# Optimization experiments

Measured on AMD Instinct MI355X. Metric: run time of the kernel, lower is better.

The kernel has to match this reference:

```python
import jax, jax.numpy as jnp
import numpy as np

FACTOR = 5  # init arg 'factor'


def setup_inputs() -> dict:
    key = jax.random.key(0)
    ks = jax.random.split(key, 9)
    B, L, H, D = 32, 4096, 8, 64
    sh = (B, L, H, D)
    scale = 0.125  # 1/sqrt(D)
    return {
        "queries": jax.random.normal(ks[0], sh, jnp.float32),
        "keys": jax.random.normal(ks[1], sh, jnp.float32),
        "values": jax.random.normal(ks[2], sh, jnp.float32),
        "Wq": jax.random.normal(ks[3], (1, D), jnp.float32) * scale,
        "bq": jax.random.normal(ks[4], (1,), jnp.float32) * scale,
        "Wk": jax.random.normal(ks[5], (1, D), jnp.float32) * scale,
        "bk": jax.random.normal(ks[6], (1,), jnp.float32) * scale,
        "Wv": jax.random.normal(ks[7], (1, D), jnp.float32) * scale,
        "bv": jax.random.normal(ks[8], (1,), jnp.float32) * scale,
    }


def reference(queries, keys, values, Wq, bq, Wk, bk, Wv, bv):
    B, L_Q, H, D = queries.shape
    # transpose(2,1) + LazyLinear(1) + squeeze  ->  scalar series per (b, h, t)
    q = jnp.einsum('blhd,d->bhl', queries, Wq[0]) + bq[0]  # [B,H,L_Q]
    k = jnp.einsum('blhd,d->bhl', keys, Wk[0]) + bk[0]
    v = jnp.einsum('blhd,d->bhl', values, Wv[0]) + bv[0]
    # L_K == L_Q here: torch takes the last L_Q steps (identity in this config)
    k = k[:, :, -L_Q:]
    v = v[:, :, -L_Q:]
    # FFT cross-correlation scores (rfft with n=2L-1 -> L bins; irfft default -> 2L-2)
    n_fft = 2 * L_Q - 1
    Qf = jnp.fft.rfft(q, n_fft)
    Kf = jnp.conj(jnp.fft.rfft(k, n_fft))
    score = jnp.fft.irfft(Qf * Kf)[:, :, :L_Q] / L_Q  # [B,H,L_Q]
    kk = FACTOR * int(np.ceil(np.log(L_Q)))  # 45 for L_Q=4096
    weight, top_idx = jax.lax.top_k(score, kk)  # [B,H,kk]
    weight = jax.nn.softmax(weight, axis=-1)
    # torch: indices = L_Q - top_idx - 1; rolled-V row j is roll(v, j+1),
    # i.e. shift = L_Q - top_idx, so V_sel[b,h,d,t] = v[b,h,(t + top_idx[b,h,d]) % L_Q].
    t = jnp.arange(L_Q)
    gidx = (top_idx[..., None] + t[None, None, None, :]) % L_Q  # [B,H,kk,L_Q]
    V_sel = jnp.take_along_axis(v[:, :, None, :], gidx, axis=-1)  # [B,H,kk,L_Q]
    out = jnp.einsum('bhd,bhdl->bhl', weight, V_sel)  # [B,H,L_Q]
    return out[..., None]  # [B,H,L_Q,1]
```

## Files before the change

### kernel.cpp

```cpp
#include <hip/hip_runtime.h>
#include <math.h>
#include <float.h>

#define L_   4096
#define M_   8192
#define H_   8
#define D_   64
#define KK   45

#define WS_C   0
#define WS_D   4096
#define WS_TW  8192
#define WS_H1  16384
#define WS_H2  24576
#define WS_QKV 32768

__device__ __forceinline__ float2 cadd(float2 a, float2 b) { return make_float2(a.x + b.x, a.y + b.y); }
__device__ __forceinline__ float2 csub(float2 a, float2 b) { return make_float2(a.x - b.x, a.y - b.y); }
__device__ __forceinline__ float2 cmulf(float2 a, float2 b) {
  return make_float2(a.x * b.x - a.y * b.y, a.x * b.y + a.y * b.x);
}
__device__ __forceinline__ float2 cmulcf(float2 a, float2 b) {
  return make_float2(a.x * b.x + a.y * b.y, a.y * b.x - a.x * b.y);
}

__device__ __forceinline__ float2 twf(int e) {
  float s, c;
  __sincosf((float)e * -7.66990394e-4f, &s, &c);
  return make_float2(c, s);
}

#define R4DIF(BUF) { \
  const float2 a = BUF[i0], b = BUF[i0 + q], c = BUF[i0 + 2 * q], d = BUF[i0 + 3 * q]; \
  const float2 t0 = cadd(a, c), t1 = csub(a, c), t2 = cadd(b, d), t3 = csub(b, d); \
  BUF[i0]         = cadd(t0, t2); \
  BUF[i0 + q]     = cmulf(make_float2(t1.x + t3.y, t1.y - t3.x), w1); \
  BUF[i0 + 2 * q] = cmulf(csub(t0, t2), w2); \
  BUF[i0 + 3 * q] = cmulf(make_float2(t1.x - t3.y, t1.y + t3.x), w3); }

#define R4DIT(BUF) { \
  const float2 z0 = BUF[i0]; \
  const float2 z1 = cmulcf(BUF[i0 + q],     w1); \
  const float2 z2 = cmulcf(BUF[i0 + 2 * q], w2); \
  const float2 z3 = cmulcf(BUF[i0 + 3 * q], w3); \
  const float2 t0 = cadd(z0, z2), t1 = csub(z0, z2), t2 = cadd(z1, z3), u = csub(z1, z3); \
  BUF[i0]         = cadd(t0, t2); \
  BUF[i0 + q]     = make_float2(t1.x - u.y, t1.y + u.x); \
  BUF[i0 + 2 * q] = csub(t0, t2); \
  BUF[i0 + 3 * q] = make_float2(t1.x + u.y, t1.y - u.x); }

__device__ __forceinline__ float4 midpair(float4 a, float4 h) {
  float2 u = make_float2(a.x + a.z, a.y + a.w);
  float2 v = make_float2(a.x - a.z, a.y - a.w);
  u = cmulf(u, make_float2(h.x, h.y));
  v = cmulf(v, make_float2(h.z, h.w));
  return make_float4(u.x + v.x, u.y + v.y, u.x - v.x, u.y - v.y);
}

static __device__ void conv2(float2* A, float2* B, const float2* __restrict__ Hf) {
  const int tid = threadIdx.x;
  #pragma unroll
  for (int s = 0; s < 6; ++s) {
    const int q = 2048 >> (2 * s);
    __syncthreads();
    #pragma unroll
    for (int r = 0; r < 2; ++r) {
      const int bid = tid + (r << 10);
      const int j   = bid & (q - 1);
      const int i0  = ((bid >> (11 - 2 * s)) << (13 - 2 * s)) + j;
      const float2 w1 = twf(j << (2 * s));
      const float2 w2 = cmulf(w1, w1);
      const float2 w3 = cmulf(w2, w1);
      R4DIF(A) R4DIF(B)
    }
  }
  __syncthreads();
  #pragma unroll
  for (int r = 0; r < 4; ++r) {
    const int p = tid + (r << 10);
    const float4 h = reinterpret_cast<const float4*>(Hf)[p];
    reinterpret_cast<float4*>(A)[p] = midpair(reinterpret_cast<float4*>(A)[p], h);
    reinterpret_cast<float4*>(B)[p] = midpair(reinterpret_cast<float4*>(B)[p], h);
  }
  #pragma unroll
  for (int s = 5; s >= 0; --s) {
    const int q = 2048 >> (2 * s);
    __syncthreads();
    #pragma unroll
    for (int r = 0; r < 2; ++r) {
      const int bid = tid + (r << 10);
      const int j   = bid & (q - 1);
      const int i0  = ((bid >> (11 - 2 * s)) << (13 - 2 * s)) + j;
      const float2 w1 = twf(j << (2 * s));
      const float2 w2 = cmulf(w1, w1);
      const float2 w3 = cmulf(w2, w1);
      R4DIT(A) R4DIT(B)
    }
  }
  __syncthreads();
}

static __device__ void conv1(float2* A, const float2* __restrict__ Hf) {
  const int tid = threadIdx.x;
  #pragma unroll
  for (int s = 0; s < 6; ++s) {
    const int q = 2048 >> (2 * s);
    __syncthreads();
    #pragma unroll
    for (int r = 0; r < 2; ++r) {
      const int bid = tid + (r << 10);
      const int j   = bid & (q - 1);
      const int i0  = ((bid >> (11 - 2 * s)) << (13 - 2 * s)) + j;
      const float2 w1 = twf(j << (2 * s));
      const float2 w2 = cmulf(w1, w1);
      const float2 w3 = cmulf(w2, w1);
      R4DIF(A)
    }
  }
  __syncthreads();
  #pragma unroll
  for (int r = 0; r < 4; ++r) {
    const int p = tid + (r << 10);
    const float4 h = reinterpret_cast<const float4*>(Hf)[p];
    reinterpret_cast<float4*>(A)[p] = midpair(reinterpret_cast<float4*>(A)[p], h);
  }
  #pragma unroll
  for (int s = 5; s >= 0; --s) {
    const int q = 2048 >> (2 * s);
    __syncthreads();
    #pragma unroll
    for (int r = 0; r < 2; ++r) {
      const int bid = tid + (r << 10);
      const int j   = bid & (q - 1);
      const int i0  = ((bid >> (11 - 2 * s)) << (13 - 2 * s)) + j;
      const float2 w1 = twf(j << (2 * s));
      const float2 w2 = cmulf(w1, w1);
      const float2 w3 = cmulf(w2, w1);
      R4DIT(A)
    }
  }
  __syncthreads();
}

template <int NT>
static __device__ void fft_dif_tab(float2* buf, const float2* __restrict__ tw) {
  const int tid = threadIdx.x;
  for (int s = 0; s < 6; ++s) {
    const int q = 2048 >> (2 * s);
    __syncthreads();
    for (int r = 0; r < 2048 / NT; ++r) {
      const int bid = tid + r * NT;
      const int j   = bid & (q - 1);
      const int i0  = ((bid >> (11 - 2 * s)) << (13 - 2 * s)) + j;
      const int e   = j << (2 * s);
      const float2 w1 = tw[e], w2 = tw[2 * e], w3 = tw[3 * e];
      R4DIF(buf)
    }
  }
  __syncthreads();
  for (int r = 0; r < 4096 / NT; ++r) {
    const int i0 = (tid + r * NT) << 1;
    const float2 a = buf[i0], b = buf[i0 + 1];
    buf[i0] = cadd(a, b); buf[i0 + 1] = csub(a, b);
  }
  __syncthreads();
}

extern "C" __global__ void setup_tables(float2* ws) {
  const int idx = blockIdx.x * 512 + threadIdx.x;
  if (idx < 4096) {
    const long p = ((long)idx * idx) % 16382;
    const double th = -M_PI * (double)p / 8191.0;
    double s, c; sincos(th, &s, &c);
    ws[WS_C + idx] = make_float2((float)c, (float)s);
  } else if (idx < 8192) {
    const int j = idx - 4096;
    const long p = ((long)j * j) % 16380;
    const double th = M_PI * (double)p / 8190.0;
    double s, c; sincos(th, &s, &c);
    ws[WS_D + j] = make_float2((float)c, (float)s);
  } else if (idx < 16384) {
    const int j = idx - 8192;
    const double th = -M_PI * (double)j / 4096.0;
    double s, c; sincos(th, &s, &c);
    ws[WS_TW + j] = make_float2((float)c, (float)s);
  }
}

extern "C" __global__ __launch_bounds__(512, 1) void setup_filters(float2* ws) {
  __shared__ __align__(16) float2 buf[M_];
  const float2* src = ws + (blockIdx.x == 0 ? WS_C : WS_D);
  float2*       dst = ws + (blockIdx.x == 0 ? WS_H1 : WS_H2);
  const float2* tw  = ws + WS_TW;
  for (int i = threadIdx.x; i < M_; i += 512) {
    float2 val = make_float2(0.f, 0.f);
    if (i != 4096) {
      const int jj = (i <= 4095) ? i : (M_ - i);
      const float2 e = src[jj];
      val = make_float2(e.x, -e.y);
    }
    buf[i] = val;
  }
  fft_dif_tab<512>(buf, tw);
  const float sc = 1.0f / 8192.0f;
  for (int i = threadIdx.x; i < M_; i += 512)
    dst[i] = make_float2(buf[i].x * sc, buf[i].y * sc);
}

#define PROJ_ISSUE(BUF, IT) { \
  const int s_ = (IT) >> 3, g_ = (IT) & 7; \
  const int l0_ = lbase + (wave << 1) + (g_ << 3); \
  const float4* p_ = (s_ == 0 ? q4p : (s_ == 1 ? k4p : v4p)) + (((size_t)l0_) << 7) + (lane << 2); \
  BUF[0] = p_[0]; \
  BUF[1] = p_[1]; \
  BUF[2] = p_[2]; \
  BUF[3] = p_[3]; }

#define PROJ_REDUCE(BUF, IT) { \
  const int s_ = (IT) >> 3, g_ = (IT) & 7; \
  const int l0_ = lbase + (wave << 1) + (g_ << 3); \
  const float4 w0_ = (s_ == 0 ? wq0 : (s_ == 1 ? wk0 : wv0)); \
  const float4 w1_ = (s_ == 0 ? wq1 : (s_ == 1 ? wk1 : wv1)); \
  const float4 w2_ = (s_ == 0 ? wq2 : (s_ == 1 ? wk2 : wv2)); \
  const float4 w3_ = (s_ == 0 ? wq3 : (s_ == 1 ? wk3 : wv3)); \
  float f_ = BUF[0].x * w0_.x + BUF[0].y * w0_.y + BUF[0].z * w0_.z + BUF[0].w * w0_.w \
           + BUF[1].x * w1_.x + BUF[1].y * w1_.y + BUF[1].z * w1_.z + BUF[1].w * w1_.w \
           + BUF[2].x * w2_.x + BUF[2].y * w2_.y + BUF[2].z * w2_.z + BUF[2].w * w2_.w \
           + BUF[3].x * w3_.x + BUF[3].y * w3_.y + BUF[3].z * w3_.z + BUF[3].w * w3_.w; \
  f_ += __shfl_xor(f_, 1); f_ += __shfl_xor(f_, 2); \
  if (qt == 0) { \
    float* d_ = (s_ == 0 ? q_ws : (s_ == 1 ? k_ws : v_ws)) + (((size_t)(b8 + hh)) << 12) + l0_ + dl; \
    *d_ = f_ + (s_ == 0 ? bq0 : (s_ == 1 ? bk0 : bv0)); } }

extern "C" __global__ __launch_bounds__(256, 4)
void proj_kernel(const float* __restrict__ queries, const float* __restrict__ keys,
                 const float* __restrict__ values,
                 const float* __restrict__ Wq, const float* __restrict__ bq,
                 const float* __restrict__ Wk, const float* __restrict__ bk,
                 const float* __restrict__ Wv, const float* __restrict__ bv,
                 float* __restrict__ q_ws, float* __restrict__ k_ws,
                 float* __restrict__ v_ws)
{
  const int tid  = threadIdx.x;
  const int wave = tid >> 6;
  const int lane = tid & 63;
  const int qt   = lane & 3;
  const int rr   = lane >> 2;
  const int hh   = rr & 7;
  const int dl   = rr >> 3;
  const int blk  = blockIdx.x;
  const int b    = blk >> 6;
  const int b8   = b * 8;
  const int lbase = (blk & 63) << 6;

  const float4* q4p = reinterpret_cast<const float4*>(queries) + (size_t)b * 524288;
  const float4* k4p = reinterpret_cast<const float4*>(keys)    + (size_t)b * 524288;
  const float4* v4p = reinterpret_cast<const float4*>(values)  + (size_t)b * 524288;

  const float4* Wq4 = reinterpret_cast<const float4*>(Wq);
  const float4* Wk4 = reinterpret_cast<const float4*>(Wk);
  const float4* Wv4 = reinterpret_cast<const float4*>(Wv);
  const float4 wq0 = Wq4[qt * 4 + 0], wq1 = Wq4[qt * 4 + 1], wq2 = Wq4[qt * 4 + 2], wq3 = Wq4[qt * 4 + 3];
  const float4 wk0 = Wk4[qt * 4 + 0], wk1 = Wk4[qt * 4 + 1], wk2 = Wk4[qt * 4 + 2], wk3 = Wk4[qt * 4 + 3];
  const float4 wv0 = Wv4[qt * 4 + 0], wv1 = Wv4[qt * 4 + 1], wv2 = Wv4[qt * 4 + 2], wv3 = Wv4[qt * 4 + 3];
  const float bq0 = bq[0], bk0 = bk[0], bv0 = bv[0];

  float4 bA[4], bB[4], bC[4];
  PROJ_ISSUE(bA, 0)
  PROJ_ISSUE(bB, 1)
  #pragma unroll
  for (int it = 0; it < 24; ++it) {
    const int nx = it + 2;
    if (nx < 24) {
      if      (nx % 3 == 0) { PROJ_ISSUE(bA, nx) }
      else if (nx % 3 == 1) { PROJ_ISSUE(bB, nx) }
      else                  { PROJ_ISSUE(bC, nx) }
    }
    if      (it % 3 == 0) { PROJ_REDUCE(bA, it) }
    else if (it % 3 == 1) { PROJ_REDUCE(bB, it) }
    else                  { PROJ_REDUCE(bC, it) }
  }
}

extern "C" __global__ __launch_bounds__(1024, 1)
void autocorr_main(const float2* __restrict__ ws,
                   const float* __restrict__ q_ws, const float* __restrict__ k_ws,
                   const float* __restrict__ v_ws, float* __restrict__ outp)
{
  __shared__ __align__(16) float2 bufA[M_];
  __shared__ __align__(16) float2 bufB[M_];
  __shared__ float  v_lds[L_];
  __shared__ float  cand_v[16 * KK];
  __shared__ int    cand_i[16 * KK];
  __shared__ float  w_sh[KK];
  __shared__ int    i_sh[KK];

  const int tid = threadIdx.x;
  const int bh  = blockIdx.x;

  const float2* c_t = ws + WS_C;
  const float2* d_t = ws + WS_D;
  const float2* H1  = ws + WS_H1;
  const float2* H2  = ws + WS_H2;
  const float* qrow = q_ws + ((size_t)bh << 12);
  const float* krow = k_ws + ((size_t)bh << 12);
  const float* vrow = v_ws + ((size_t)bh << 12);

  {
    const float4 v4 = reinterpret_cast<const float4*>(vrow)[tid];
    reinterpret_cast<float4*>(v_lds)[tid] = v4;
    const float4 k4 = reinterpret_cast<const float4*>(krow)[tid];
    const float4 q4 = reinterpret_cast<const float4*>(qrow)[tid];
    const float4 c01 = reinterpret_cast<const float4*>(c_t)[2 * tid];
    const float4 c23 = reinterpret_cast<const float4*>(c_t)[2 * tid + 1];
    float4* A4 = reinterpret_cast<float4*>(bufA);
    float4* B4 = reinterpret_cast<float4*>(bufB);
    A4[2 * tid]     = make_float4(k4.x * c01.x, k4.x * c01.y, k4.y * c01.z, k4.y * c01.w);
    A4[2 * tid + 1] = make_float4(k4.z * c23.x, k4.z * c23.y, k4.w * c23.z, k4.w * c23.w);
    B4[2 * tid]     = make_float4(q4.x * c01.x, q4.x * c01.y, q4.y * c01.z, q4.y * c01.w);
    B4[2 * tid + 1] = make_float4(q4.z * c23.x, q4.z * c23.y, q4.w * c23.z, q4.w * c23.w);
    const float4 z = make_float4(0.f, 0.f, 0.f, 0.f);
    A4[2048 + tid] = z; A4[3072 + tid] = z;
    B4[2048 + tid] = z; B4[3072 + tid] = z;
  }

  conv2(bufA, bufB, H1);

  #pragma unroll
  for (int r = 0; r < 4; ++r) {
    const int m = tid + (r << 10);
    const float2 cc = c_t[m];
    const float2 K = cmulf(cc, bufA[m]);
    const float2 Q = cmulf(cc, bufB[m]);
    const float2 F = cmulcf(Q, K);
    float2 g;
    if (m == 0 || m == 4095) g = make_float2(F.x, 0.f);
    else                     g = make_float2(2.f * F.x, 2.f * F.y);
    bufA[m] = cmulf(g, d_t[m]);
  }
  #pragma unroll
  for (int r = 4; r < 8; ++r) bufA[tid + (r << 10)] = make_float2(0.f, 0.f);

  conv1(bufA, H2);

  const float SCALE = (float)(1.0 / (8190.0 * 4096.0));
  float svv[4]; int sii[4];
  #pragma unroll
  for (int r = 0; r < 4; ++r) {
    const int t = tid + (r << 10);
    const float2 Z = cmulf(d_t[t], bufA[t]);
    svv[r] = Z.x * SCALE;
    sii[r] = t;
  }
  const int lane = tid & 63, wv = tid >> 6;
  for (int it = 0; it < KK; ++it) {
    float bvv = -FLT_MAX; int bii = 0x7fffffff;
    #pragma unroll
    for (int c = 0; c < 4; ++c)
      if (svv[c] > bvv || (svv[c] == bvv && sii[c] < bii)) { bvv = svv[c]; bii = sii[c]; }
    #pragma unroll
    for (int off = 1; off < 64; off <<= 1) {
      const float ov = __shfl_xor(bvv, off);
      const int   oi = __shfl_xor(bii, off);
      if (ov > bvv || (ov == bvv && oi < bii)) { bvv = ov; bii = oi; }
    }
    #pragma unroll
    for (int c = 0; c < 4; ++c) if (sii[c] == bii) svv[c] = -FLT_MAX;
    if (lane == 0) { cand_v[wv * KK + it] = bvv; cand_i[wv * KK + it] = bii; }
  }
  __syncthreads();

  if (tid < 64) {
    float mv[12]; int mi[12];
    #pragma unroll
    for (int c = 0; c < 12; ++c) {
      const int id = tid + 64 * c;
      if (id < 16 * KK) { mv[c] = cand_v[id]; mi[c] = cand_i[id]; }
      else              { mv[c] = -FLT_MAX;   mi[c] = 0x7fffffff; }
    }
    float m0 = 0.f, sum = 0.f, myv = -FLT_MAX; int myi = 0;
    for (int it = 0; it < KK; ++it) {
      float bvv = -FLT_MAX; int bii = 0x7fffffff;
      #pragma unroll
      for (int c = 0; c < 12; ++c)
        if (mv[c] > bvv || (mv[c] == bvv && mi[c] < bii)) { bvv = mv[c]; bii = mi[c]; }
      #pragma unroll
      for (int off = 1; off < 64; off <<= 1) {
        const float ov = __shfl_xor(bvv, off);
        const int   oi = __shfl_xor(bii, off);
        if (ov > bvv || (ov == bvv && oi < bii)) { bvv = ov; bii = oi; }
      }
      if (it == 0) m0 = bvv;
      sum += expf(bvv - m0);
      if (tid == it) { myv = bvv; myi = bii; }
      #pragma unroll
      for (int c = 0; c < 12; ++c) if (mi[c] == bii) mv[c] = -FLT_MAX;
    }
    if (tid < KK) { w_sh[tid] = expf(myv - m0) / sum; i_sh[tid] = myi; }
  }
  __syncthreads();

  {
    float acc[4] = {0, 0, 0, 0};
    for (int j = 0; j < KK; ++j) {
      const float wj = w_sh[j];
      const int   bse = i_sh[j] + tid;
      #pragma unroll
      for (int r = 0; r < 4; ++r)
        acc[r] = fmaf(wj, v_lds[(bse + (r << 10)) & (L_ - 1)], acc[r]);
    }
    float* op = outp + ((size_t)bh << 12);
    #pragma unroll
    for (int r = 0; r < 4; ++r) op[tid + (r << 10)] = acc[r];
  }
}

extern "C" void kernel_launch(void* const* d_in, const int* in_sizes, int n_in,
                              void* d_out, int out_size, void* d_ws, size_t ws_size,
                              hipStream_t stream) {
  const float* queries = (const float*)d_in[0];
  const float* keys    = (const float*)d_in[1];
  const float* values  = (const float*)d_in[2];
  const float* Wq = (const float*)d_in[3];
  const float* bq = (const float*)d_in[4];
  const float* Wk = (const float*)d_in[5];
  const float* bk = (const float*)d_in[6];
  const float* Wv = (const float*)d_in[7];
  const float* bv = (const float*)d_in[8];
  float2* ws = (float2*)d_ws;
  float* q_ws = (float*)d_ws + 2 * WS_QKV;
  float* k_ws = q_ws + (1 << 20);
  float* v_ws = k_ws + (1 << 20);
  float* out = (float*)d_out;

  hipLaunchKernelGGL(setup_tables,  dim3(32), dim3(512), 0, stream, ws);
  hipLaunchKernelGGL(setup_filters, dim3(2),  dim3(512), 0, stream, ws);
  hipLaunchKernelGGL(proj_kernel,   dim3(2048), dim3(256), 0, stream,
                     queries, keys, values, Wq, bq, Wk, bk, Wv, bv, q_ws, k_ws, v_ws);
  hipLaunchKernelGGL(autocorr_main, dim3(256), dim3(1024), 0, stream,
                     ws, q_ws, k_ws, v_ws, out);
}
```

Before: 339.9 us.

## Replace radix-4 FFT convolutions with radix-8 stages and fused middle stage

Rewrites the Bluestein convolution FFTs from six radix-4 stages to three radix-8 stages plus a fused 'megamid' stage, which does the last radix-8 forward pass, the filter multiply and the first inverse pass in registers. The first forward stage is fused with loading the inputs and the chirp premultiply, and skips the known zero padding. This halves the number of shared-memory passes and __syncthreads barriers per convolution. Each thread holds more registers and uses more twiddle multiplies. The launch-bounds minimum-blocks hint also changes from 1 to 4.

```diff
diff --git a/kernel.cpp b/kernel.cpp
--- a/kernel.cpp
+++ b/kernel.cpp
@@ -30,140 +30,143 @@
   return make_float2(c, s);
 }
 
-#define R4DIF(BUF) { \
-  const float2 a = BUF[i0], b = BUF[i0 + q], c = BUF[i0 + 2 * q], d = BUF[i0 + 3 * q]; \
-  const float2 t0 = cadd(a, c), t1 = csub(a, c), t2 = cadd(b, d), t3 = csub(b, d); \
-  BUF[i0]         = cadd(t0, t2); \
-  BUF[i0 + q]     = cmulf(make_float2(t1.x + t3.y, t1.y - t3.x), w1); \
-  BUF[i0 + 2 * q] = cmulf(csub(t0, t2), w2); \
-  BUF[i0 + 3 * q] = cmulf(make_float2(t1.x - t3.y, t1.y + t3.x), w3); }
-
-#define R4DIT(BUF) { \
-  const float2 z0 = BUF[i0]; \
-  const float2 z1 = cmulcf(BUF[i0 + q],     w1); \
-  const float2 z2 = cmulcf(BUF[i0 + 2 * q], w2); \
-  const float2 z3 = cmulcf(BUF[i0 + 3 * q], w3); \
-  const float2 t0 = cadd(z0, z2), t1 = csub(z0, z2), t2 = cadd(z1, z3), u = csub(z1, z3); \
-  BUF[i0]         = cadd(t0, t2); \
-  BUF[i0 + q]     = make_float2(t1.x - u.y, t1.y + u.x); \
-  BUF[i0 + 2 * q] = csub(t0, t2); \
-  BUF[i0 + 3 * q] = make_float2(t1.x + u.y, t1.y - u.x); }
-
-__device__ __forceinline__ float4 midpair(float4 a, float4 h) {
-  float2 u = make_float2(a.x + a.z, a.y + a.w);
-  float2 v = make_float2(a.x - a.z, a.y - a.w);
-  u = cmulf(u, make_float2(h.x, h.y));
-  v = cmulf(v, make_float2(h.z, h.w));
-  return make_float4(u.x + v.x, u.y + v.y, u.x - v.x, u.y - v.y);
-}
-
-static __device__ void conv2(float2* A, float2* B, const float2* __restrict__ Hf) {
-  const int tid = threadIdx.x;
-  #pragma unroll
-  for (int s = 0; s < 6; ++s) {
-    const int q = 2048 >> (2 * s);
-    __syncthreads();
-    #pragma unroll
-    for (int r = 0; r < 2; ++r) {
-      const int bid = tid + (r << 10);
-      const int j   = bid & (q - 1);
-      const int i0  = ((bid >> (11 - 2 * s)) << (13 - 2 * s)) + j;
-      const float2 w1 = twf(j << (2 * s));
-      const float2 w2 = cmulf(w1, w1);
-      const float2 w3 = cmulf(w2, w1);
-      R4DIF(A) R4DIF(B)
-    }
-  }
-  __syncthreads();
-  #pragma unroll
-  for (int r = 0; r < 4; ++r) {
-    const int p = tid + (r << 10);
-    const float4 h = reinterpret_cast<const float4*>(Hf)[p];
-    reinterpret_cast<float4*>(A)[p] = midpair(reinterpret_cast<float4*>(A)[p], h);
-    reinterpret_cast<float4*>(B)[p] = midpair(reinterpret_cast<float4*>(B)[p], h);
-  }
-  #pragma unroll
-  for (int s = 5; s >= 0; --s) {
-    const int q = 2048 >> (2 * s);
-    __syncthreads();
-    #pragma unroll
-    for (int r = 0; r < 2; ++r) {
-      const int bid = tid + (r << 10);
-      const int j   = bid & (q - 1);
-      const int i0  = ((bid >> (11 - 2 * s)) << (13 - 2 * s)) + j;
-      const float2 w1 = twf(j << (2 * s));
-      const float2 w2 = cmulf(w1, w1);
-      const float2 w3 = cmulf(w2, w1);
-      R4DIT(A) R4DIT(B)
-    }
-  }
-  __syncthreads();
-}
-
-static __device__ void conv1(float2* A, const float2* __restrict__ Hf) {
-  const int tid = threadIdx.x;
-  #pragma unroll
-  for (int s = 0; s < 6; ++s) {
-    const int q = 2048 >> (2 * s);
-    __syncthreads();
-    #pragma unroll
-    for (int r = 0; r < 2; ++r) {
-      const int bid = tid + (r << 10);
-      const int j   = bid & (q - 1);
-      const int i0  = ((bid >> (11 - 2 * s)) << (13 - 2 * s)) + j;
-      const float2 w1 = twf(j << (2 * s));
-      const float2 w2 = cmulf(w1, w1);
-      const float2 w3 = cmulf(w2, w1);
-      R4DIF(A)
-    }
-  }
-  __syncthreads();
-  #pragma unroll
-  for (int r = 0; r < 4; ++r) {
-    const int p = tid + (r << 10);
-    const float4 h = reinterpret_cast<const float4*>(Hf)[p];
-    reinterpret_cast<float4*>(A)[p] = midpair(reinterpret_cast<float4*>(A)[p], h);
-  }
-  #pragma unroll
-  for (int s = 5; s >= 0; --s) {
-    const int q = 2048 >> (2 * s);
-    __syncthreads();
-    #pragma unroll
-    for (int r = 0; r < 2; ++r) {
-      const int bid = tid + (r << 10);
-      const int j   = bid & (q - 1);
-      const int i0  = ((bid >> (11 - 2 * s)) << (13 - 2 * s)) + j;
-      const float2 w1 = twf(j << (2 * s));
-      const float2 w2 = cmulf(w1, w1);
-      const float2 w3 = cmulf(w2, w1);
-      R4DIT(A)
-    }
-  }
-  __syncthreads();
-}
-
-template <int NT>
-static __device__ void fft_dif_tab(float2* buf, const float2* __restrict__ tw) {
-  const int tid = threadIdx.x;
-  for (int s = 0; s < 6; ++s) {
-    const int q = 2048 >> (2 * s);
-    __syncthreads();
-    for (int r = 0; r < 2048 / NT; ++r) {
-      const int bid = tid + r * NT;
-      const int j   = bid & (q - 1);
-      const int i0  = ((bid >> (11 - 2 * s)) << (13 - 2 * s)) + j;
-      const int e   = j << (2 * s);
-      const float2 w1 = tw[e], w2 = tw[2 * e], w3 = tw[3 * e];
-      R4DIF(buf)
-    }
-  }
-  __syncthreads();
-  for (int r = 0; r < 4096 / NT; ++r) {
-    const int i0 = (tid + r * NT) << 1;
-    const float2 a = buf[i0], b = buf[i0 + 1];
-    buf[i0] = cadd(a, b); buf[i0 + 1] = csub(a, b);
-  }
-  __syncthreads();
+__device__ __forceinline__ void mk_tw(int e, float2 w[8]) {
+  w[1] = twf(e);
+  w[2] = cmulf(w[1], w[1]);
+  w[3] = cmulf(w[2], w[1]);
+  w[4] = cmulf(w[2], w[2]);
+  w[5] = cmulf(w[4], w[1]);
+  w[6] = cmulf(w[3], w[3]);
+  w[7] = cmulf(w[4], w[3]);
+}
+
+__device__ __forceinline__ void bfly8_dif(float2 x[8]) {
+  const float2 a0 = cadd(x[0], x[4]), a1 = csub(x[0], x[4]);
+  const float2 a2 = cadd(x[2], x[6]), a3 = csub(x[2], x[6]);
+  const float2 a4 = cadd(x[1], x[5]), a5 = csub(x[1], x[5]);
+  const float2 a6 = cadd(x[3], x[7]), a7 = csub(x[3], x[7]);
+  const float2 b0 = cadd(a0, a2), b1 = csub(a0, a2);
+  const float2 b2 = cadd(a4, a6), b3 = csub(a4, a6);
+  const float s = 0.70710678118654752f;
+  const float2 c0 = make_float2(a1.x + a3.y, a1.y - a3.x);
+  const float2 c1 = make_float2(a1.x - a3.y, a1.y + a3.x);
+  const float2 c2 = make_float2(a5.x + a7.y, a5.y - a7.x);
+  const float2 c3 = make_float2(a5.x - a7.y, a5.y + a7.x);
+  const float2 t2 = make_float2(s * (c2.x + c2.y), s * (c2.y - c2.x));
+  const float2 t3 = make_float2(s * (c3.y - c3.x), -s * (c3.x + c3.y));
+  x[0] = cadd(b0, b2);
+  x[4] = csub(b0, b2);
+  x[2] = make_float2(b1.x + b3.y, b1.y - b3.x);
+  x[6] = make_float2(b1.x - b3.y, b1.y + b3.x);
+  x[1] = cadd(c0, t2);
+  x[5] = csub(c0, t2);
+  x[3] = cadd(c1, t3);
+  x[7] = csub(c1, t3);
+}
+
+__device__ __forceinline__ void bfly8_dit(float2 x[8]) {
+  const float2 a0 = cadd(x[0], x[4]), a1 = csub(x[0], x[4]);
+  const float2 a2 = cadd(x[2], x[6]), a3 = csub(x[2], x[6]);
+  const float2 a4 = cadd(x[1], x[5]), a5 = csub(x[1], x[5]);
+  const float2 a6 = cadd(x[3], x[7]), a7 = csub(x[3], x[7]);
+  const float2 b0 = cadd(a0, a2), b1 = csub(a0, a2);
+  const float2 b2 = cadd(a4, a6), b3 = csub(a4, a6);
+  const float s = 0.70710678118654752f;
+  const float2 c0 = make_float2(a1.x - a3.y, a1.y + a3.x);
+  const float2 c1 = make_float2(a1.x + a3.y, a1.y - a3.x);
+  const float2 c2 = make_float2(a5.x - a7.y, a5.y + a7.x);
+  const float2 c3 = make_float2(a5.x + a7.y, a5.y - a7.x);
+  const float2 t2 = make_float2(s * (c2.x - c2.y), s * (c2.x + c2.y));
+  const float2 t3 = make_float2(-s * (c3.x + c3.y), s * (c3.x - c3.y));
+  x[0] = cadd(b0, b2);
+  x[4] = csub(b0, b2);
+  x[2] = make_float2(b1.x - b3.y, b1.y + b3.x);
+  x[6] = make_float2(b1.x + b3.y, b1.y - b3.x);
+  x[1] = cadd(c0, t2);
+  x[5] = csub(c0, t2);
+  x[3] = cadd(c1, t3);
+  x[7] = csub(c1, t3);
+}
+
+#define C8f 0.923879532511287f
+#define S8f 0.382683432365090f
+#define Q8f 0.707106781186548f
+
+__device__ __forceinline__ void megamid(float2* T, const float2* __restrict__ Hf, int wk) {
+  float4* T4 = reinterpret_cast<float4*>(T);
+  const float4* H4 = reinterpret_cast<const float4*>(Hf);
+  const int b4 = wk << 3;
+  const int st = wk & 7;
+  float2 ev[8], od[8];
+  #pragma unroll
+  for (int mm = 0; mm < 8; ++mm) {
+    const int m = (mm + st) & 7;
+    const float4 t = T4[b4 + m];
+    ev[m] = make_float2(t.x, t.y);
+    od[m] = make_float2(t.z, t.w);
+  }
+  bfly8_dif(ev);
+  bfly8_dif(od);
+  od[1] = cmulf(od[1], make_float2(C8f, -S8f));
+  od[2] = cmulf(od[2], make_float2(Q8f, -Q8f));
+  od[3] = cmulf(od[3], make_float2(S8f, -C8f));
+  od[4] = make_float2(od[4].y, -od[4].x);
+  od[5] = cmulf(od[5], make_float2(-S8f, -C8f));
+  od[6] = cmulf(od[6], make_float2(-Q8f, -Q8f));
+  od[7] = cmulf(od[7], make_float2(-C8f, -S8f));
+  #pragma unroll
+  for (int m = 0; m < 8; ++m) {
+    const float4 h = H4[b4 + m];
+    float2 u = cadd(ev[m], od[m]);
+    float2 v = csub(ev[m], od[m]);
+    u = cmulf(u, make_float2(h.x, h.y));
+    v = cmulf(v, make_float2(h.z, h.w));
+    ev[m] = cadd(u, v);
+    od[m] = csub(u, v);
+  }
+  od[1] = cmulcf(od[1], make_float2(C8f, -S8f));
+  od[2] = cmulcf(od[2], make_float2(Q8f, -Q8f));
+  od[3] = cmulcf(od[3], make_float2(S8f, -C8f));
+  od[4] = make_float2(-od[4].y, od[4].x);
+  od[5] = cmulcf(od[5], make_float2(-S8f, -C8f));
+  od[6] = cmulcf(od[6], make_float2(-Q8f, -Q8f));
+  od[7] = cmulcf(od[7], make_float2(-C8f, -S8f));
+  bfly8_dit(ev);
+  bfly8_dit(od);
+  #pragma unroll
+  for (int mm = 0; mm < 8; ++mm) {
+    const int m = (mm + st) & 7;
+    T4[b4 + m] = make_float4(ev[m].x, ev[m].y, od[m].x, od[m].y);
+  }
+}
+
+__device__ __forceinline__ void r8_fwd_stage(float2* T, int s, int tid) {
+  const int q  = 1024 >> (3 * s);
+  const int j  = tid & (q - 1);
+  const int i0 = ((tid >> (10 - 3 * s)) << (13 - 3 * s)) + j;
+  float2 w[8]; mk_tw(j << (3 * s), w);
+  float2 x[8];
+  #pragma unroll
+  for (int k = 0; k < 8; ++k) x[k] = T[i0 + k * q];
+  bfly8_dif(x);
+  T[i0] = x[0];
+  #pragma unroll
+  for (int k = 1; k < 8; ++k) T[i0 + k * q] = cmulf(x[k], w[k]);
+}
+
+__device__ __forceinline__ void r8_inv_stage(float2* T, int s, int tid) {
+  const int q  = 1024 >> (3 * s);
+  const int j  = tid & (q - 1);
+  const int i0 = ((tid >> (10 - 3 * s)) << (13 - 3 * s)) + j;
+  float2 w[8]; mk_tw(j << (3 * s), w);
+  float2 x[8];
+  #pragma unroll
+  for (int k = 0; k < 8; ++k) x[k] = T[i0 + k * q];
+  #pragma unroll
+  for (int k = 1; k < 8; ++k) x[k] = cmulcf(x[k], w[k]);
+  bfly8_dit(x);
+  #pragma unroll
+  for (int k = 0; k < 8; ++k) T[i0 + k * q] = x[k];
 }
 
 extern "C" __global__ void setup_tables(float2* ws) {
@@ -187,6 +190,35 @@
   }
 }
 
+template <int NT>
+static __device__ void fft8_dif_tab(float2* buf, const float2* __restrict__ tw) {
+  const int tid = threadIdx.x;
+  for (int s = 0; s < 4; ++s) {
+    const int q = 1024 >> (3 * s);
+    __syncthreads();
+    for (int r = 0; r < 1024 / NT; ++r) {
+      const int bid = tid + r * NT;
+      const int j   = bid & (q - 1);
+      const int i0  = ((bid >> (10 - 3 * s)) << (13 - 3 * s)) + j;
+      const int e   = j << (3 * s);
+      float2 x[8];
+      #pragma unroll
+      for (int k = 0; k < 8; ++k) x[k] = buf[i0 + k * q];
+      bfly8_dif(x);
+      buf[i0] = x[0];
+      #pragma unroll
+      for (int k = 1; k < 8; ++k) buf[i0 + k * q] = cmulf(x[k], tw[k * e]);
+    }
+  }
+  __syncthreads();
+  for (int r = 0; r < 4096 / NT; ++r) {
+    const int i0 = (tid + r * NT) << 1;
+    const float2 a = buf[i0], b = buf[i0 + 1];
+    buf[i0] = cadd(a, b); buf[i0 + 1] = csub(a, b);
+  }
+  __syncthreads();
+}
+
 extern "C" __global__ __launch_bounds__(512, 1) void setup_filters(float2* ws) {
   __shared__ __align__(16) float2 buf[M_];
   const float2* src = ws + (blockIdx.x == 0 ? WS_C : WS_D);
@@ -201,7 +233,7 @@
     }
     buf[i] = val;
   }
-  fft_dif_tab<512>(buf, tw);
+  fft8_dif_tab<512>(buf, tw);
   const float sc = 1.0f / 8192.0f;
   for (int i = threadIdx.x; i < M_; i += 512)
     dst[i] = make_float2(buf[i].x * sc, buf[i].y * sc);
@@ -282,7 +314,7 @@
   }
 }
 
-extern "C" __global__ __launch_bounds__(1024, 1)
+extern "C" __global__ __launch_bounds__(1024, 4)
 void autocorr_main(const float2* __restrict__ ws,
                    const float* __restrict__ q_ws, const float* __restrict__ k_ws,
                    const float* __restrict__ v_ws, float* __restrict__ outp)
@@ -309,39 +341,81 @@
   {
     const float4 v4 = reinterpret_cast<const float4*>(vrow)[tid];
     reinterpret_cast<float4*>(v_lds)[tid] = v4;
-    const float4 k4 = reinterpret_cast<const float4*>(krow)[tid];
-    const float4 q4 = reinterpret_cast<const float4*>(qrow)[tid];
-    const float4 c01 = reinterpret_cast<const float4*>(c_t)[2 * tid];
-    const float4 c23 = reinterpret_cast<const float4*>(c_t)[2 * tid + 1];
-    float4* A4 = reinterpret_cast<float4*>(bufA);
-    float4* B4 = reinterpret_cast<float4*>(bufB);
-    A4[2 * tid]     = make_float4(k4.x * c01.x, k4.x * c01.y, k4.y * c01.z, k4.y * c01.w);
-    A4[2 * tid + 1] = make_float4(k4.z * c23.x, k4.z * c23.y, k4.w * c23.z, k4.w * c23.w);
-    B4[2 * tid]     = make_float4(q4.x * c01.x, q4.x * c01.y, q4.y * c01.z, q4.y * c01.w);
-    B4[2 * tid + 1] = make_float4(q4.z * c23.x, q4.z * c23.y, q4.w * c23.z, q4.w * c23.w);
-    const float4 z = make_float4(0.f, 0.f, 0.f, 0.f);
-    A4[2048 + tid] = z; A4[3072 + tid] = z;
-    B4[2048 + tid] = z; B4[3072 + tid] = z;
-  }
-
-  conv2(bufA, bufB, H1);
-
-  #pragma unroll
-  for (int r = 0; r < 4; ++r) {
-    const int m = tid + (r << 10);
-    const float2 cc = c_t[m];
-    const float2 K = cmulf(cc, bufA[m]);
-    const float2 Q = cmulf(cc, bufB[m]);
-    const float2 F = cmulcf(Q, K);
-    float2 g;
-    if (m == 0 || m == 4095) g = make_float2(F.x, 0.f);
-    else                     g = make_float2(2.f * F.x, 2.f * F.y);
-    bufA[m] = cmulf(g, d_t[m]);
-  }
-  #pragma unroll
-  for (int r = 4; r < 8; ++r) bufA[tid + (r << 10)] = make_float2(0.f, 0.f);
-
-  conv1(bufA, H2);
+  }
+
+  {
+    float2 w[8]; mk_tw(tid, w);
+    float2 xA[8], xB[8];
+    #pragma unroll
+    for (int k = 0; k < 4; ++k) {
+      const int m = tid + (k << 10);
+      const float2 cc = c_t[m];
+      const float kv = krow[m];
+      const float qv = qrow[m];
+      xA[k] = make_float2(kv * cc.x, kv * cc.y);
+      xB[k] = make_float2(qv * cc.x, qv * cc.y);
+    }
+    #pragma unroll
+    for (int k = 4; k < 8; ++k) { xA[k] = make_float2(0.f, 0.f); xB[k] = make_float2(0.f, 0.f); }
+    bfly8_dif(xA);
+    bfly8_dif(xB);
+    bufA[tid] = xA[0];
+    bufB[tid] = xB[0];
+    #pragma unroll
+    for (int k = 1; k < 8; ++k) {
+      bufA[tid + (k << 10)] = cmulf(xA[k], w[k]);
+      bufB[tid + (k << 10)] = cmulf(xB[k], w[k]);
+    }
+  }
+  __syncthreads();
+  r8_fwd_stage(bufA, 1, tid); r8_fwd_stage(bufB, 1, tid);
+  __syncthreads();
+  r8_fwd_stage(bufA, 2, tid); r8_fwd_stage(bufB, 2, tid);
+  __syncthreads();
+  megamid((tid >> 9) ? bufB : bufA, H1, tid & 511);
+  __syncthreads();
+  r8_inv_stage(bufA, 2, tid); r8_inv_stage(bufB, 2, tid);
+  __syncthreads();
+  r8_inv_stage(bufA, 1, tid); r8_inv_stage(bufB, 1, tid);
+  __syncthreads();
+  r8_inv_stage(bufA, 0, tid); r8_inv_stage(bufB, 0, tid);
+  __syncthreads();
+
+  {
+    float2 w[8]; mk_tw(tid, w);
+    float2 x[8];
+    #pragma unroll
+    for (int k = 0; k < 4; ++k) {
+      const int m = tid + (k << 10);
+      const float2 cc = c_t[m];
+      const float2 K = cmulf(cc, bufA[m]);
+      const float2 Q = cmulf(cc, bufB[m]);
+      const float2 F = cmulcf(Q, K);
+      float2 g;
+      if (m == 0 || m == 4095) g = make_float2(F.x, 0.f);
+      else                     g = make_float2(2.f * F.x, 2.f * F.y);
+      x[k] = cmulf(g, d_t[m]);
+    }
+    #pragma unroll
+    for (int k = 4; k < 8; ++k) x[k] = make_float2(0.f, 0.f);
+    bfly8_dif(x);
+    bufA[tid] = x[0];
+    #pragma unroll
+    for (int k = 1; k < 8; ++k) bufA[tid + (k << 10)] = cmulf(x[k], w[k]);
+  }
+  __syncthreads();
+  r8_fwd_stage(bufA, 1, tid);
+  __syncthreads();
+  r8_fwd_stage(bufA, 2, tid);
+  __syncthreads();
+  if (tid < 512) megamid(bufA, H2, tid);
+  __syncthreads();
+  r8_inv_stage(bufA, 2, tid);
+  __syncthreads();
+  r8_inv_stage(bufA, 1, tid);
+  __syncthreads();
+  r8_inv_stage(bufA, 0, tid);
+  __syncthreads();
 
   const float SCALE = (float)(1.0 / (8190.0 * 4096.0));
   float svv[4]; int sii[4];
```

Measured after the change: 413.3 us. +21.6%, slower.

## Fuse first and last radix-4 FFT stages into register-resident prologue and epilogue

Applied to the files above, without the earlier changes.

Peels the first DIF stage and the last DIT stage out of each Bluestein convolution and runs them in registers, fused with the chirp premultiply, the zero padding, the spectrum product, and the score extraction. Half of each butterfly's inputs are known zeros, so the peeled first stage skips those loads. The inverse pass only keeps the outputs that are needed. This cuts several shared-memory round trips, barriers and zero-fill stores per block. The cost is more register pressure, and the global loads of k and q become scalar instead of float4.

```diff
diff --git a/kernel.cpp b/kernel.cpp
--- a/kernel.cpp
+++ b/kernel.cpp
@@ -49,6 +49,26 @@
   BUF[i0 + 2 * q] = csub(t0, t2); \
   BUF[i0 + 3 * q] = make_float2(t1.x + u.y, t1.y - u.x); }
 
+__device__ __forceinline__ void bfly4_dif(float2 x[4], float2 w1, float2 w2, float2 w3) {
+  const float2 t0 = cadd(x[0], x[2]), t1 = csub(x[0], x[2]);
+  const float2 t2 = cadd(x[1], x[3]), t3 = csub(x[1], x[3]);
+  x[0] = cadd(t0, t2);
+  x[1] = cmulf(make_float2(t1.x + t3.y, t1.y - t3.x), w1);
+  x[2] = cmulf(csub(t0, t2), w2);
+  x[3] = cmulf(make_float2(t1.x - t3.y, t1.y + t3.x), w3);
+}
+__device__ __forceinline__ void bfly4_dit(float2 x[4], float2 w1, float2 w2, float2 w3) {
+  const float2 z0 = x[0];
+  const float2 z1 = cmulcf(x[1], w1);
+  const float2 z2 = cmulcf(x[2], w2);
+  const float2 z3 = cmulcf(x[3], w3);
+  const float2 t0 = cadd(z0, z2), t1 = csub(z0, z2), t2 = cadd(z1, z3), u = csub(z1, z3);
+  x[0] = cadd(t0, t2);
+  x[1] = make_float2(t1.x - u.y, t1.y + u.x);
+  x[2] = csub(t0, t2);
+  x[3] = make_float2(t1.x + u.y, t1.y - u.x);
+}
+
 __device__ __forceinline__ float4 midpair(float4 a, float4 h) {
   float2 u = make_float2(a.x + a.z, a.y + a.w);
   float2 v = make_float2(a.x - a.z, a.y - a.w);
@@ -57,10 +77,10 @@
   return make_float4(u.x + v.x, u.y + v.y, u.x - v.x, u.y - v.y);
 }
 
-static __device__ void conv2(float2* A, float2* B, const float2* __restrict__ Hf) {
+static __device__ void fwd_stages2(float2* A, float2* B) {
   const int tid = threadIdx.x;
   #pragma unroll
-  for (int s = 0; s < 6; ++s) {
+  for (int s = 1; s < 6; ++s) {
     const int q = 2048 >> (2 * s);
     __syncthreads();
     #pragma unroll
@@ -74,16 +94,11 @@
       R4DIF(A) R4DIF(B)
     }
   }
-  __syncthreads();
-  #pragma unroll
-  for (int r = 0; r < 4; ++r) {
-    const int p = tid + (r << 10);
-    const float4 h = reinterpret_cast<const float4*>(Hf)[p];
-    reinterpret_cast<float4*>(A)[p] = midpair(reinterpret_cast<float4*>(A)[p], h);
-    reinterpret_cast<float4*>(B)[p] = midpair(reinterpret_cast<float4*>(B)[p], h);
-  }
-  #pragma unroll
-  for (int s = 5; s >= 0; --s) {
+}
+static __device__ void inv_stages2(float2* A, float2* B) {
+  const int tid = threadIdx.x;
+  #pragma unroll
+  for (int s = 5; s >= 1; --s) {
     const int q = 2048 >> (2 * s);
     __syncthreads();
     #pragma unroll
@@ -97,13 +112,11 @@
       R4DIT(A) R4DIT(B)
     }
   }
-  __syncthreads();
-}
-
-static __device__ void conv1(float2* A, const float2* __restrict__ Hf) {
+}
+static __device__ void fwd_stages1(float2* A) {
   const int tid = threadIdx.x;
   #pragma unroll
-  for (int s = 0; s < 6; ++s) {
+  for (int s = 1; s < 6; ++s) {
     const int q = 2048 >> (2 * s);
     __syncthreads();
     #pragma unroll
@@ -117,15 +130,11 @@
       R4DIF(A)
     }
   }
-  __syncthreads();
-  #pragma unroll
-  for (int r = 0; r < 4; ++r) {
-    const int p = tid + (r << 10);
-    const float4 h = reinterpret_cast<const float4*>(Hf)[p];
-    reinterpret_cast<float4*>(A)[p] = midpair(reinterpret_cast<float4*>(A)[p], h);
-  }
-  #pragma unroll
-  for (int s = 5; s >= 0; --s) {
+}
+static __device__ void inv_stages1(float2* A) {
+  const int tid = threadIdx.x;
+  #pragma unroll
+  for (int s = 5; s >= 1; --s) {
     const int q = 2048 >> (2 * s);
     __syncthreads();
     #pragma unroll
@@ -139,7 +148,6 @@
       R4DIT(A)
     }
   }
-  __syncthreads();
 }
 
 template <int NT>
@@ -309,49 +317,115 @@
   {
     const float4 v4 = reinterpret_cast<const float4*>(vrow)[tid];
     reinterpret_cast<float4*>(v_lds)[tid] = v4;
-    const float4 k4 = reinterpret_cast<const float4*>(krow)[tid];
-    const float4 q4 = reinterpret_cast<const float4*>(qrow)[tid];
-    const float4 c01 = reinterpret_cast<const float4*>(c_t)[2 * tid];
-    const float4 c23 = reinterpret_cast<const float4*>(c_t)[2 * tid + 1];
-    float4* A4 = reinterpret_cast<float4*>(bufA);
-    float4* B4 = reinterpret_cast<float4*>(bufB);
-    A4[2 * tid]     = make_float4(k4.x * c01.x, k4.x * c01.y, k4.y * c01.z, k4.y * c01.w);
-    A4[2 * tid + 1] = make_float4(k4.z * c23.x, k4.z * c23.y, k4.w * c23.z, k4.w * c23.w);
-    B4[2 * tid]     = make_float4(q4.x * c01.x, q4.x * c01.y, q4.y * c01.z, q4.y * c01.w);
-    B4[2 * tid + 1] = make_float4(q4.z * c23.x, q4.z * c23.y, q4.w * c23.z, q4.w * c23.w);
-    const float4 z = make_float4(0.f, 0.f, 0.f, 0.f);
-    A4[2048 + tid] = z; A4[3072 + tid] = z;
-    B4[2048 + tid] = z; B4[3072 + tid] = z;
-  }
-
-  conv2(bufA, bufB, H1);
-
+  }
+
+  #pragma unroll
+  for (int r = 0; r < 2; ++r) {
+    const int bid = tid + (r << 10);
+    const float2 w1 = twf(bid);
+    const float2 w2 = cmulf(w1, w1);
+    const float2 w3 = cmulf(w2, w1);
+    const float2 cc0 = c_t[bid], cc1 = c_t[bid + 2048];
+    const float k0 = krow[bid], k1 = krow[bid + 2048];
+    const float q0 = qrow[bid], q1 = qrow[bid + 2048];
+    float2 xa[4] = { make_float2(k0 * cc0.x, k0 * cc0.y),
+                     make_float2(k1 * cc1.x, k1 * cc1.y),
+                     make_float2(0.f, 0.f), make_float2(0.f, 0.f) };
+    float2 xb[4] = { make_float2(q0 * cc0.x, q0 * cc0.y),
+                     make_float2(q1 * cc1.x, q1 * cc1.y),
+                     make_float2(0.f, 0.f), make_float2(0.f, 0.f) };
+    bfly4_dif(xa, w1, w2, w3);
+    bfly4_dif(xb, w1, w2, w3);
+    #pragma unroll
+    for (int k = 0; k < 4; ++k) {
+      bufA[bid + k * 2048] = xa[k];
+      bufB[bid + k * 2048] = xb[k];
+    }
+  }
+
+  fwd_stages2(bufA, bufB);
+  __syncthreads();
   #pragma unroll
   for (int r = 0; r < 4; ++r) {
-    const int m = tid + (r << 10);
-    const float2 cc = c_t[m];
-    const float2 K = cmulf(cc, bufA[m]);
-    const float2 Q = cmulf(cc, bufB[m]);
-    const float2 F = cmulcf(Q, K);
-    float2 g;
-    if (m == 0 || m == 4095) g = make_float2(F.x, 0.f);
-    else                     g = make_float2(2.f * F.x, 2.f * F.y);
-    bufA[m] = cmulf(g, d_t[m]);
-  }
-  #pragma unroll
-  for (int r = 4; r < 8; ++r) bufA[tid + (r << 10)] = make_float2(0.f, 0.f);
-
-  conv1(bufA, H2);
+    const int p = tid + (r << 10);
+    const float4 h = reinterpret_cast<const float4*>(H1)[p];
+    reinterpret_cast<float4*>(bufA)[p] = midpair(reinterpret_cast<float4*>(bufA)[p], h);
+    reinterpret_cast<float4*>(bufB)[p] = midpair(reinterpret_cast<float4*>(bufB)[p], h);
+  }
+  inv_stages2(bufA, bufB);
+  __syncthreads();
+
+  {
+    float2 gd[2][2];
+    #pragma unroll
+    for (int r = 0; r < 2; ++r) {
+      const int bid = tid + (r << 10);
+      const float2 w1 = twf(bid);
+      const float2 w2 = cmulf(w1, w1);
+      const float2 w3 = cmulf(w2, w1);
+      float2 xa[4], xb[4];
+      #pragma unroll
+      for (int k = 0; k < 4; ++k) { xa[k] = bufA[bid + k * 2048]; xb[k] = bufB[bid + k * 2048]; }
+      bfly4_dit(xa, w1, w2, w3);
+      bfly4_dit(xb, w1, w2, w3);
+      #pragma unroll
+      for (int k = 0; k < 2; ++k) {
+        const int m = bid + k * 2048;
+        const float2 cc = c_t[m];
+        const float2 K = cmulf(cc, xa[k]);
+        const float2 Q = cmulf(cc, xb[k]);
+        const float2 F = cmulcf(Q, K);
+        float2 g;
+        if (m == 0 || m == 4095) g = make_float2(F.x, 0.f);
+        else                     g = make_float2(2.f * F.x, 2.f * F.y);
+        gd[r][k] = cmulf(g, d_t[m]);
+      }
+    }
+    #pragma unroll
+    for (int r = 0; r < 2; ++r) {
+      const int bid = tid + (r << 10);
+      const float2 w1 = twf(bid);
+      const float2 w2 = cmulf(w1, w1);
+      const float2 w3 = cmulf(w2, w1);
+      float2 x[4] = { gd[r][0], gd[r][1], make_float2(0.f, 0.f), make_float2(0.f, 0.f) };
+      bfly4_dif(x, w1, w2, w3);
+      #pragma unroll
+      for (int k = 0; k < 4; ++k) bufA[bid + k * 2048] = x[k];
+    }
+  }
+
+  fwd_stages1(bufA);
+  __syncthreads();
+  #pragma unroll
+  for (int r = 0; r < 4; ++r) {
+    const int p = tid + (r << 10);
+    const float4 h = reinterpret_cast<const float4*>(H2)[p];
+    reinterpret_cast<float4*>(bufA)[p] = midpair(reinterpret_cast<float4*>(bufA)[p], h);
+  }
+  inv_stages1(bufA);
+  __syncthreads();
 
   const float SCALE = (float)(1.0 / (8190.0 * 4096.0));
   float svv[4]; int sii[4];
   #pragma unroll
-  for (int r = 0; r < 4; ++r) {
-    const int t = tid + (r << 10);
-    const float2 Z = cmulf(d_t[t], bufA[t]);
-    svv[r] = Z.x * SCALE;
-    sii[r] = t;
-  }
+  for (int r = 0; r < 2; ++r) {
+    const int bid = tid + (r << 10);
+    const float2 w1 = twf(bid);
+    const float2 w2 = cmulf(w1, w1);
+    const float2 w3 = cmulf(w2, w1);
+    float2 x[4];
+    #pragma unroll
+    for (int k = 0; k < 4; ++k) x[k] = bufA[bid + k * 2048];
+    bfly4_dit(x, w1, w2, w3);
+    #pragma unroll
+    for (int k = 0; k < 2; ++k) {
+      const int t = bid + k * 2048;
+      const float2 Z = cmulf(d_t[t], x[k]);
+      svv[2 * r + k] = Z.x * SCALE;
+      sii[2 * r + k] = t;
+    }
+  }
+
   const int lane = tid & 63, wv = tid >> 6;
   for (int it = 0; it < KK; ++it) {
     float bvv = -FLT_MAX; int bii = 0x7fffffff;
```

Result: no change. 338.9 us (-0.3%).
